# Performance work log

Hardware: AMD Instinct MI355X
Metric: run time of the kernel (lower is better)

Reference implementation:

```python
import jax, jax.numpy as jnp
import numpy as np

OFFSET_SCALE = 6.0
B, H, W = 128, 256, 256


def setup_inputs() -> dict:
    key = jax.random.key(0)
    k1, k2, k3, k4 = jax.random.split(key, 4)
    Offset = jax.random.normal(k1, (B, 3, H, W), dtype=jnp.float32)
    Posmap_kpt = jax.random.normal(k2, (B, 3, H, W), dtype=jnp.float32)
    mean_posmap = jax.random.normal(k3, (3, H, W), dtype=jnp.float32)
    uv_kpt = jax.random.randint(k4, (68, 2), 0, 256, dtype=jnp.int64)
    return {"Offset": Offset, "Posmap_kpt": Posmap_kpt,
            "mean_posmap": mean_posmap, "uv_kpt": uv_kpt}


def _kpt2tform_batch(kpt_src, kpt_dst):
    # kpt_src, kpt_dst: (B, 68, 3). Index 33 is the nose-tip anchor.
    sd1 = jnp.sum(jnp.linalg.norm(kpt_src - kpt_src[:, 33:34], axis=2), axis=1)[:, None, None]
    sd2 = jnp.sum(jnp.linalg.norm(kpt_dst - kpt_dst[:, 33:34], axis=2), axis=1)[:, None, None]
    A = kpt_src * sd2 / sd1
    Bm = kpt_dst
    AA = A - A.mean(axis=1, keepdims=True)
    BB = Bm - Bm.mean(axis=1, keepdims=True)
    Hm = jnp.einsum('bki,bkj->bij', AA, BB)  # (B, 3, 3)
    U, S, Vh = jnp.linalg.svd(Hm, full_matrices=False)
    # torch.svd returns V with H = U S V^T; R = V @ U^T
    R = jnp.einsum('bji,bkj->bik', Vh, U)
    t = jnp.mean(Bm - jnp.einsum('bki,bji->bkj', A, R), axis=1)  # (B, 3)
    return R * sd2 / sd1, t


def reference(Offset, Posmap_kpt, mean_posmap, uv_kpt):
    b = Offset.shape[0]
    offsetmap = Offset * OFFSET_SCALE + mean_posmap            # (B, 3, 256, 256)
    offsetmap = jnp.transpose(offsetmap, (0, 2, 3, 1))          # (B, 256, 256, 3)
    kptmap = jnp.transpose(Posmap_kpt, (0, 2, 3, 1))
    kpt_dst = kptmap[:, uv_kpt[:, 0], uv_kpt[:, 1]]             # (B, 68, 3)
    kpt_src = offsetmap[:, uv_kpt[:, 0], uv_kpt[:, 1]]
    offs = offsetmap.reshape(b, H * W, 3)                       # (B, 65536, 3)
    R, T = _kpt2tform_batch(kpt_src, kpt_dst)
    outpos = jnp.einsum('bki,bji->bkj', offs, R) + T[:, None, :]
    outpos = outpos.reshape(b, H, W, 3)
    return jnp.transpose(outpos, (0, 3, 1, 2))
```

## Files before the change

kernel.cpp:

```cpp
#include <hip/hip_runtime.h>
#include <math.h>

#define BATCH 128
#define HH 256
#define WW 256
#define HW (HH * WW)
#define HW4 (HW / 4)
#define NKPT 68

__device__ inline double wave_sum64(double v) {
#pragma unroll
    for (int off = 32; off > 0; off >>= 1) v += __shfl_xor(v, off);
    return v;
}

__global__ __launch_bounds__(64) void tform_kernel(
    const float* __restrict__ Offset, const float* __restrict__ Posmap,
    const float* __restrict__ meanp, const int* __restrict__ uv,
    float* __restrict__ RT) {
    const int b = blockIdx.x;
    const int lane = threadIdx.x;
    const float* offb = Offset + (size_t)b * 3 * HW;
    const float* dstb = Posmap + (size_t)b * 3 * HW;

    const bool has1 = lane < (NKPT - 64);

    double s0[3], d0[3], s1[3] = {0, 0, 0}, d1[3] = {0, 0, 0};
    {
        const int p0 = uv[lane * 2 + 0] * WW + uv[lane * 2 + 1];
#pragma unroll
        for (int i = 0; i < 3; i++) {
            s0[i] = (double)offb[(size_t)i * HW + p0] * 6.0 +
                    (double)meanp[(size_t)i * HW + p0];
            d0[i] = (double)dstb[(size_t)i * HW + p0];
        }
        if (has1) {
            const int k1 = lane + 64;
            const int p1 = uv[k1 * 2 + 0] * WW + uv[k1 * 2 + 1];
#pragma unroll
            for (int i = 0; i < 3; i++) {
                s1[i] = (double)offb[(size_t)i * HW + p1] * 6.0 +
                        (double)meanp[(size_t)i * HW + p1];
                d1[i] = (double)dstb[(size_t)i * HW + p1];
            }
        }
    }

    double s33[3], d33[3];
#pragma unroll
    for (int i = 0; i < 3; i++) {
        s33[i] = __shfl(s0[i], 33);
        d33[i] = __shfl(d0[i], 33);
    }

    double ns0 = 0, nd0 = 0, ns1 = 0, nd1 = 0;
    double ssum[3], dsum[3];
#pragma unroll
    for (int i = 0; i < 3; i++) {
        double es = s0[i] - s33[i], ed = d0[i] - d33[i];
        ns0 += es * es;
        nd0 += ed * ed;
        es = s1[i] - s33[i];
        ed = d1[i] - d33[i];
        ns1 += es * es;
        nd1 += ed * ed;
        ssum[i] = s0[i] + s1[i];
        dsum[i] = d0[i] + d1[i];
    }
    double sd1p = sqrt(ns0) + (has1 ? sqrt(ns1) : 0.0);
    double sd2p = sqrt(nd0) + (has1 ? sqrt(nd1) : 0.0);

    const double sd1 = wave_sum64(sd1p);
    const double sd2 = wave_sum64(sd2p);
#pragma unroll
    for (int i = 0; i < 3; i++) {
        ssum[i] = wave_sum64(ssum[i]);
        dsum[i] = wave_sum64(dsum[i]);
    }

    const double s = sd2 / sd1;
    double sbar[3], dbar[3];
#pragma unroll
    for (int i = 0; i < 3; i++) {
        sbar[i] = ssum[i] / NKPT;
        dbar[i] = dsum[i] / NKPT;
    }

    double Hm[3][3];
    {
        double aa0[3], bb0[3], aa1[3], bb1[3];
#pragma unroll
        for (int i = 0; i < 3; i++) {
            aa0[i] = (s0[i] - sbar[i]) * s;
            bb0[i] = d0[i] - dbar[i];
            aa1[i] = has1 ? (s1[i] - sbar[i]) * s : 0.0;
            bb1[i] = has1 ? (d1[i] - dbar[i]) : 0.0;
        }
#pragma unroll
        for (int i = 0; i < 3; i++)
#pragma unroll
            for (int j = 0; j < 3; j++)
                Hm[i][j] = wave_sum64(aa0[i] * bb0[j] + aa1[i] * bb1[j]);
    }

    if (lane != 0) return;

    double A[3][3];
    for (int i = 0; i < 3; i++)
        for (int j = 0; j < 3; j++) {
            double acc = 0;
            for (int kk = 0; kk < 3; kk++) acc += Hm[kk][i] * Hm[kk][j];
            A[i][j] = acc;
        }

    double V[3][3] = {{1, 0, 0}, {0, 1, 0}, {0, 0, 1}};
    for (int sweep = 0; sweep < 12; ++sweep) {
        double off = fabs(A[0][1]) + fabs(A[0][2]) + fabs(A[1][2]);
        double diag = fabs(A[0][0]) + fabs(A[1][1]) + fabs(A[2][2]);
        if (off <= diag * 1e-15) break;
        for (int p = 0; p < 2; p++)
            for (int q = p + 1; q < 3; q++) {
                double apq = A[p][q];
                if (fabs(apq) < 1e-300) continue;
                double theta = (A[q][q] - A[p][p]) / (2.0 * apq);
                double t = (theta >= 0.0 ? 1.0 : -1.0) /
                           (fabs(theta) + sqrt(theta * theta + 1.0));
                double c = 1.0 / sqrt(t * t + 1.0);
                double sn = t * c;
                A[p][p] -= t * apq;
                A[q][q] += t * apq;
                A[p][q] = 0.0;
                A[q][p] = 0.0;
                int r = 3 - p - q;
                double arp = A[r][p], arq = A[r][q];
                A[r][p] = A[p][r] = c * arp - sn * arq;
                A[r][q] = A[q][r] = sn * arp + c * arq;
#pragma unroll
                for (int rr = 0; rr < 3; rr++) {
                    double vrp = V[rr][p], vrq = V[rr][q];
                    V[rr][p] = c * vrp - sn * vrq;
                    V[rr][q] = sn * vrp + c * vrq;
                }
            }
    }
    double isig[3];
#pragma unroll
    for (int i = 0; i < 3; i++) {
        double l = A[i][i];
        if (l < 1e-30) l = 1e-30;
        isig[i] = 1.0 / sqrt(l);
    }
    double Wm[3][3];
    for (int i = 0; i < 3; i++)
        for (int j = 0; j < 3; j++) {
            double acc = 0;
            for (int kk = 0; kk < 3; kk++) acc += V[i][kk] * V[j][kk] * isig[kk];
            Wm[i][j] = acc;
        }
    double R[3][3];
    for (int i = 0; i < 3; i++)
        for (int j = 0; j < 3; j++) {
            double acc = 0;
            for (int kk = 0; kk < 3; kk++) acc += Wm[i][kk] * Hm[j][kk];
            R[i][j] = acc;
        }

    float* rt = RT + b * 12;
    for (int j = 0; j < 3; j++) {
        for (int i = 0; i < 3; i++) rt[j * 3 + i] = (float)(R[j][i] * s);
        double tj = dbar[j];
        for (int i = 0; i < 3; i++) tj -= s * sbar[i] * R[j][i];
        rt[9 + j] = (float)tj;
    }
}

__global__ __launch_bounds__(256) void apply_kernel(
    const float4* __restrict__ Off, const float4* __restrict__ Mean,
    const float* __restrict__ RT, float4* __restrict__ Out) {
    const int CHUNKS = HW4 / 256;
    const int b = blockIdx.x / CHUNKS;
    const int p = (blockIdx.x % CHUNKS) * 256 + threadIdx.x;

    const float* rt = RT + b * 12;
    const float r00 = rt[0], r01 = rt[1], r02 = rt[2];
    const float r10 = rt[3], r11 = rt[4], r12 = rt[5];
    const float r20 = rt[6], r21 = rt[7], r22 = rt[8];
    const float t0 = rt[9], t1 = rt[10], t2 = rt[11];

    const size_t base = (size_t)b * 3 * HW4;
    float4 o0 = Off[base + p];
    float4 o1 = Off[base + HW4 + p];
    float4 o2 = Off[base + 2 * HW4 + p];
    float4 m0 = Mean[p];
    float4 m1 = Mean[HW4 + p];
    float4 m2 = Mean[2 * HW4 + p];

    float4 y0, y1, y2;
#define APPLY(comp)                                                   \
    {                                                                 \
        float x0 = fmaf(o0.comp, 6.0f, m0.comp);                      \
        float x1 = fmaf(o1.comp, 6.0f, m1.comp);                      \
        float x2 = fmaf(o2.comp, 6.0f, m2.comp);                      \
        y0.comp = fmaf(x0, r00, fmaf(x1, r01, fmaf(x2, r02, t0)));    \
        y1.comp = fmaf(x0, r10, fmaf(x1, r11, fmaf(x2, r12, t1)));    \
        y2.comp = fmaf(x0, r20, fmaf(x1, r21, fmaf(x2, r22, t2)));    \
    }
    APPLY(x)
    APPLY(y)
    APPLY(z)
    APPLY(w)
#undef APPLY

    Out[base + p] = y0;
    Out[base + HW4 + p] = y1;
    Out[base + 2 * HW4 + p] = y2;
}

extern "C" void kernel_launch(void* const* d_in, const int* in_sizes, int n_in,
                              void* d_out, int out_size, void* d_ws,
                              size_t ws_size, hipStream_t stream) {
    const float* Offset = (const float*)d_in[0];
    const float* Posmap = (const float*)d_in[1];
    const float* meanp = (const float*)d_in[2];
    const int* uv = (const int*)d_in[3];
    float* out = (float*)d_out;
    float* RT = (float*)d_ws;

    tform_kernel<<<BATCH, 64, 0, stream>>>(Offset, Posmap, meanp, uv, RT);
    apply_kernel<<<BATCH * (HW4 / 256), 256, 0, stream>>>(
        (const float4*)Offset, (const float4*)meanp, RT, (float4*)out);
}
```

Baseline: 44.00 us.

## Fuse per-batch transform solve into apply kernel with redundant per-block computation

Merges the two kernels into one. Every 256-thread block now recomputes the batch's Procrustes transform in its first wave (keypoint gather, wave reductions, Jacobi SVD on lane 0) and passes it to the rest of the block through shared memory. The block's Offset loads are issued before the solve so they overlap it. The change also switches the output writes to nontemporal stores. It removes the second launch and the workspace round trip, but repeats the serial double-precision solve 64 times per batch and makes every block wait at a barrier for it.

Result: slower. 83.73 us (+90.3%).

```diff
diff --git a/kernel.cpp b/kernel.cpp
--- a/kernel.cpp
+++ b/kernel.cpp
@@ -6,7 +6,10 @@
 #define WW 256
 #define HW (HH * WW)
 #define HW4 (HW / 4)
+#define CHUNKS (HW4 / 256)
 #define NKPT 68
+
+typedef float fx4 __attribute__((ext_vector_type(4)));
 
 __device__ inline double wave_sum64(double v) {
 #pragma unroll
@@ -14,206 +17,202 @@
     return v;
 }
 
-__global__ __launch_bounds__(64) void tform_kernel(
+__global__ __launch_bounds__(256, 4) void fused_kernel(
     const float* __restrict__ Offset, const float* __restrict__ Posmap,
     const float* __restrict__ meanp, const int* __restrict__ uv,
-    float* __restrict__ RT) {
-    const int b = blockIdx.x;
-    const int lane = threadIdx.x;
-    const float* offb = Offset + (size_t)b * 3 * HW;
-    const float* dstb = Posmap + (size_t)b * 3 * HW;
-
-    const bool has1 = lane < (NKPT - 64);
-
-    double s0[3], d0[3], s1[3] = {0, 0, 0}, d1[3] = {0, 0, 0};
-    {
-        const int p0 = uv[lane * 2 + 0] * WW + uv[lane * 2 + 1];
-#pragma unroll
-        for (int i = 0; i < 3; i++) {
-            s0[i] = (double)offb[(size_t)i * HW + p0] * 6.0 +
-                    (double)meanp[(size_t)i * HW + p0];
-            d0[i] = (double)dstb[(size_t)i * HW + p0];
-        }
-        if (has1) {
-            const int k1 = lane + 64;
-            const int p1 = uv[k1 * 2 + 0] * WW + uv[k1 * 2 + 1];
-#pragma unroll
-            for (int i = 0; i < 3; i++) {
-                s1[i] = (double)offb[(size_t)i * HW + p1] * 6.0 +
-                        (double)meanp[(size_t)i * HW + p1];
-                d1[i] = (double)dstb[(size_t)i * HW + p1];
-            }
-        }
-    }
-
-    double s33[3], d33[3];
-#pragma unroll
-    for (int i = 0; i < 3; i++) {
-        s33[i] = __shfl(s0[i], 33);
-        d33[i] = __shfl(d0[i], 33);
-    }
-
-    double ns0 = 0, nd0 = 0, ns1 = 0, nd1 = 0;
-    double ssum[3], dsum[3];
-#pragma unroll
-    for (int i = 0; i < 3; i++) {
-        double es = s0[i] - s33[i], ed = d0[i] - d33[i];
-        ns0 += es * es;
-        nd0 += ed * ed;
-        es = s1[i] - s33[i];
-        ed = d1[i] - d33[i];
-        ns1 += es * es;
-        nd1 += ed * ed;
-        ssum[i] = s0[i] + s1[i];
-        dsum[i] = d0[i] + d1[i];
-    }
-    double sd1p = sqrt(ns0) + (has1 ? sqrt(ns1) : 0.0);
-    double sd2p = sqrt(nd0) + (has1 ? sqrt(nd1) : 0.0);
-
-    const double sd1 = wave_sum64(sd1p);
-    const double sd2 = wave_sum64(sd2p);
-#pragma unroll
-    for (int i = 0; i < 3; i++) {
-        ssum[i] = wave_sum64(ssum[i]);
-        dsum[i] = wave_sum64(dsum[i]);
-    }
-
-    const double s = sd2 / sd1;
-    double sbar[3], dbar[3];
-#pragma unroll
-    for (int i = 0; i < 3; i++) {
-        sbar[i] = ssum[i] / NKPT;
-        dbar[i] = dsum[i] / NKPT;
-    }
-
-    double Hm[3][3];
-    {
-        double aa0[3], bb0[3], aa1[3], bb1[3];
-#pragma unroll
-        for (int i = 0; i < 3; i++) {
-            aa0[i] = (s0[i] - sbar[i]) * s;
-            bb0[i] = d0[i] - dbar[i];
-            aa1[i] = has1 ? (s1[i] - sbar[i]) * s : 0.0;
-            bb1[i] = has1 ? (d1[i] - dbar[i]) : 0.0;
-        }
-#pragma unroll
-        for (int i = 0; i < 3; i++)
-#pragma unroll
-            for (int j = 0; j < 3; j++)
-                Hm[i][j] = wave_sum64(aa0[i] * bb0[j] + aa1[i] * bb1[j]);
-    }
-
-    if (lane != 0) return;
-
-    double A[3][3];
-    for (int i = 0; i < 3; i++)
-        for (int j = 0; j < 3; j++) {
-            double acc = 0;
-            for (int kk = 0; kk < 3; kk++) acc += Hm[kk][i] * Hm[kk][j];
-            A[i][j] = acc;
-        }
-
-    double V[3][3] = {{1, 0, 0}, {0, 1, 0}, {0, 0, 1}};
-    for (int sweep = 0; sweep < 12; ++sweep) {
-        double off = fabs(A[0][1]) + fabs(A[0][2]) + fabs(A[1][2]);
-        double diag = fabs(A[0][0]) + fabs(A[1][1]) + fabs(A[2][2]);
-        if (off <= diag * 1e-15) break;
-        for (int p = 0; p < 2; p++)
-            for (int q = p + 1; q < 3; q++) {
-                double apq = A[p][q];
-                if (fabs(apq) < 1e-300) continue;
-                double theta = (A[q][q] - A[p][p]) / (2.0 * apq);
-                double t = (theta >= 0.0 ? 1.0 : -1.0) /
-                           (fabs(theta) + sqrt(theta * theta + 1.0));
-                double c = 1.0 / sqrt(t * t + 1.0);
-                double sn = t * c;
-                A[p][p] -= t * apq;
-                A[q][q] += t * apq;
-                A[p][q] = 0.0;
-                A[q][p] = 0.0;
-                int r = 3 - p - q;
-                double arp = A[r][p], arq = A[r][q];
-                A[r][p] = A[p][r] = c * arp - sn * arq;
-                A[r][q] = A[q][r] = sn * arp + c * arq;
-#pragma unroll
-                for (int rr = 0; rr < 3; rr++) {
-                    double vrp = V[rr][p], vrq = V[rr][q];
-                    V[rr][p] = c * vrp - sn * vrq;
-                    V[rr][q] = sn * vrp + c * vrq;
-                }
-            }
-    }
-    double isig[3];
-#pragma unroll
-    for (int i = 0; i < 3; i++) {
-        double l = A[i][i];
-        if (l < 1e-30) l = 1e-30;
-        isig[i] = 1.0 / sqrt(l);
-    }
-    double Wm[3][3];
-    for (int i = 0; i < 3; i++)
-        for (int j = 0; j < 3; j++) {
-            double acc = 0;
-            for (int kk = 0; kk < 3; kk++) acc += V[i][kk] * V[j][kk] * isig[kk];
-            Wm[i][j] = acc;
-        }
-    double R[3][3];
-    for (int i = 0; i < 3; i++)
-        for (int j = 0; j < 3; j++) {
-            double acc = 0;
-            for (int kk = 0; kk < 3; kk++) acc += Wm[i][kk] * Hm[j][kk];
-            R[i][j] = acc;
-        }
-
-    float* rt = RT + b * 12;
-    for (int j = 0; j < 3; j++) {
-        for (int i = 0; i < 3; i++) rt[j * 3 + i] = (float)(R[j][i] * s);
-        double tj = dbar[j];
-        for (int i = 0; i < 3; i++) tj -= s * sbar[i] * R[j][i];
-        rt[9 + j] = (float)tj;
-    }
-}
-
-__global__ __launch_bounds__(256) void apply_kernel(
-    const float4* __restrict__ Off, const float4* __restrict__ Mean,
-    const float* __restrict__ RT, float4* __restrict__ Out) {
-    const int CHUNKS = HW4 / 256;
+    float* __restrict__ Out) {
+    __shared__ float rt_s[12];
+
     const int b = blockIdx.x / CHUNKS;
     const int p = (blockIdx.x % CHUNKS) * 256 + threadIdx.x;
-
-    const float* rt = RT + b * 12;
-    const float r00 = rt[0], r01 = rt[1], r02 = rt[2];
-    const float r10 = rt[3], r11 = rt[4], r12 = rt[5];
-    const float r20 = rt[6], r21 = rt[7], r22 = rt[8];
-    const float t0 = rt[9], t1 = rt[10], t2 = rt[11];
-
-    const size_t base = (size_t)b * 3 * HW4;
-    float4 o0 = Off[base + p];
-    float4 o1 = Off[base + HW4 + p];
-    float4 o2 = Off[base + 2 * HW4 + p];
-    float4 m0 = Mean[p];
-    float4 m1 = Mean[HW4 + p];
-    float4 m2 = Mean[2 * HW4 + p];
-
-    float4 y0, y1, y2;
-#define APPLY(comp)                                                   \
-    {                                                                 \
-        float x0 = fmaf(o0.comp, 6.0f, m0.comp);                      \
-        float x1 = fmaf(o1.comp, 6.0f, m1.comp);                      \
-        float x2 = fmaf(o2.comp, 6.0f, m2.comp);                      \
-        y0.comp = fmaf(x0, r00, fmaf(x1, r01, fmaf(x2, r02, t0)));    \
-        y1.comp = fmaf(x0, r10, fmaf(x1, r11, fmaf(x2, r12, t1)));    \
-        y2.comp = fmaf(x0, r20, fmaf(x1, r21, fmaf(x2, r22, t2)));    \
+    const size_t base4 = (size_t)b * 3 * HW4;
+
+    const fx4* Off4 = (const fx4*)Offset;
+    fx4 o0 = Off4[base4 + p];
+    fx4 o1 = Off4[base4 + HW4 + p];
+    fx4 o2 = Off4[base4 + 2 * HW4 + p];
+
+    if (threadIdx.x < 64) {
+        const int lane = threadIdx.x;
+        const float* offb = Offset + (size_t)b * 3 * HW;
+        const float* dstb = Posmap + (size_t)b * 3 * HW;
+        const bool has1 = lane < (NKPT - 64);
+
+        double s0[3], d0[3], s1[3] = {0, 0, 0}, d1[3] = {0, 0, 0};
+        {
+            const int p0 = uv[lane * 2 + 0] * WW + uv[lane * 2 + 1];
+#pragma unroll
+            for (int i = 0; i < 3; i++) {
+                s0[i] = (double)offb[(size_t)i * HW + p0] * 6.0 +
+                        (double)meanp[(size_t)i * HW + p0];
+                d0[i] = (double)dstb[(size_t)i * HW + p0];
+            }
+            if (has1) {
+                const int k1 = lane + 64;
+                const int p1 = uv[k1 * 2 + 0] * WW + uv[k1 * 2 + 1];
+#pragma unroll
+                for (int i = 0; i < 3; i++) {
+                    s1[i] = (double)offb[(size_t)i * HW + p1] * 6.0 +
+                            (double)meanp[(size_t)i * HW + p1];
+                    d1[i] = (double)dstb[(size_t)i * HW + p1];
+                }
+            }
+        }
+
+        double s33[3], d33[3];
+#pragma unroll
+        for (int i = 0; i < 3; i++) {
+            s33[i] = __shfl(s0[i], 33);
+            d33[i] = __shfl(d0[i], 33);
+        }
+
+        double ns0 = 0, nd0 = 0, ns1 = 0, nd1 = 0;
+        double ssum[3], dsum[3];
+#pragma unroll
+        for (int i = 0; i < 3; i++) {
+            double es = s0[i] - s33[i], ed = d0[i] - d33[i];
+            ns0 += es * es;
+            nd0 += ed * ed;
+            es = s1[i] - s33[i];
+            ed = d1[i] - d33[i];
+            ns1 += es * es;
+            nd1 += ed * ed;
+            ssum[i] = s0[i] + s1[i];
+            dsum[i] = d0[i] + d1[i];
+        }
+        double sd1p = sqrt(ns0) + (has1 ? sqrt(ns1) : 0.0);
+        double sd2p = sqrt(nd0) + (has1 ? sqrt(nd1) : 0.0);
+
+        const double sd1 = wave_sum64(sd1p);
+        const double sd2 = wave_sum64(sd2p);
+#pragma unroll
+        for (int i = 0; i < 3; i++) {
+            ssum[i] = wave_sum64(ssum[i]);
+            dsum[i] = wave_sum64(dsum[i]);
+        }
+
+        const double s = sd2 / sd1;
+        double sbar[3], dbar[3];
+#pragma unroll
+        for (int i = 0; i < 3; i++) {
+            sbar[i] = ssum[i] / NKPT;
+            dbar[i] = dsum[i] / NKPT;
+        }
+
+        double Hm[3][3];
+        {
+            double aa0[3], bb0[3], aa1[3], bb1[3];
+#pragma unroll
+            for (int i = 0; i < 3; i++) {
+                aa0[i] = (s0[i] - sbar[i]) * s;
+                bb0[i] = d0[i] - dbar[i];
+                aa1[i] = has1 ? (s1[i] - sbar[i]) * s : 0.0;
+                bb1[i] = has1 ? (d1[i] - dbar[i]) : 0.0;
+            }
+#pragma unroll
+            for (int i = 0; i < 3; i++)
+#pragma unroll
+                for (int j = 0; j < 3; j++)
+                    Hm[i][j] = wave_sum64(aa0[i] * bb0[j] + aa1[i] * bb1[j]);
+        }
+
+        if (lane == 0) {
+            double A[3][3];
+            for (int i = 0; i < 3; i++)
+                for (int j = 0; j < 3; j++) {
+                    double acc = 0;
+                    for (int kk = 0; kk < 3; kk++) acc += Hm[kk][i] * Hm[kk][j];
+                    A[i][j] = acc;
+                }
+
+            double V[3][3] = {{1, 0, 0}, {0, 1, 0}, {0, 0, 1}};
+            for (int sweep = 0; sweep < 12; ++sweep) {
+                double off = fabs(A[0][1]) + fabs(A[0][2]) + fabs(A[1][2]);
+                double diag = fabs(A[0][0]) + fabs(A[1][1]) + fabs(A[2][2]);
+                if (off <= diag * 1e-15) break;
+                for (int pp = 0; pp < 2; pp++)
+                    for (int q = pp + 1; q < 3; q++) {
+                        double apq = A[pp][q];
+                        if (fabs(apq) < 1e-300) continue;
+                        double theta = (A[q][q] - A[pp][pp]) / (2.0 * apq);
+                        double t = (theta >= 0.0 ? 1.0 : -1.0) /
+                                   (fabs(theta) + sqrt(theta * theta + 1.0));
+                        double c = 1.0 / sqrt(t * t + 1.0);
+                        double sn = t * c;
+                        A[pp][pp] -= t * apq;
+                        A[q][q] += t * apq;
+                        A[pp][q] = 0.0;
+                        A[q][pp] = 0.0;
+                        int r = 3 - pp - q;
+                        double arp = A[r][pp], arq = A[r][q];
+                        A[r][pp] = A[pp][r] = c * arp - sn * arq;
+                        A[r][q] = A[q][r] = sn * arp + c * arq;
+#pragma unroll
+                        for (int rr = 0; rr < 3; rr++) {
+                            double vrp = V[rr][pp], vrq = V[rr][q];
+                            V[rr][pp] = c * vrp - sn * vrq;
+                            V[rr][q] = sn * vrp + c * vrq;
+                        }
+                    }
+            }
+            double isig[3];
+#pragma unroll
+            for (int i = 0; i < 3; i++) {
+                double l = A[i][i];
+                if (l < 1e-30) l = 1e-30;
+                isig[i] = 1.0 / sqrt(l);
+            }
+            double Wm[3][3];
+            for (int i = 0; i < 3; i++)
+                for (int j = 0; j < 3; j++) {
+                    double acc = 0;
+                    for (int kk = 0; kk < 3; kk++)
+                        acc += V[i][kk] * V[j][kk] * isig[kk];
+                    Wm[i][j] = acc;
+                }
+            double R[3][3];
+            for (int i = 0; i < 3; i++)
+                for (int j = 0; j < 3; j++) {
+                    double acc = 0;
+                    for (int kk = 0; kk < 3; kk++) acc += Wm[i][kk] * Hm[j][kk];
+                    R[i][j] = acc;
+                }
+            for (int j = 0; j < 3; j++) {
+                for (int i = 0; i < 3; i++)
+                    rt_s[j * 3 + i] = (float)(R[j][i] * s);
+                double tj = dbar[j];
+                for (int i = 0; i < 3; i++) tj -= s * sbar[i] * R[j][i];
+                rt_s[9 + j] = (float)tj;
+            }
+        }
     }
-    APPLY(x)
-    APPLY(y)
-    APPLY(z)
-    APPLY(w)
-#undef APPLY
-
-    Out[base + p] = y0;
-    Out[base + HW4 + p] = y1;
-    Out[base + 2 * HW4 + p] = y2;
+    __syncthreads();
+
+    const float r00 = rt_s[0], r01 = rt_s[1], r02 = rt_s[2];
+    const float r10 = rt_s[3], r11 = rt_s[4], r12 = rt_s[5];
+    const float r20 = rt_s[6], r21 = rt_s[7], r22 = rt_s[8];
+    const float t0 = rt_s[9], t1 = rt_s[10], t2 = rt_s[11];
+
+    const fx4* Mean4 = (const fx4*)meanp;
+    fx4 m0 = Mean4[p];
+    fx4 m1 = Mean4[HW4 + p];
+    fx4 m2 = Mean4[2 * HW4 + p];
+
+    fx4 y0, y1, y2;
+#pragma unroll
+    for (int c = 0; c < 4; c++) {
+        float x0 = fmaf(o0[c], 6.0f, m0[c]);
+        float x1 = fmaf(o1[c], 6.0f, m1[c]);
+        float x2 = fmaf(o2[c], 6.0f, m2[c]);
+        y0[c] = fmaf(x0, r00, fmaf(x1, r01, fmaf(x2, r02, t0)));
+        y1[c] = fmaf(x0, r10, fmaf(x1, r11, fmaf(x2, r12, t1)));
+        y2[c] = fmaf(x0, r20, fmaf(x1, r21, fmaf(x2, r22, t2)));
+    }
+
+    fx4* Out4 = (fx4*)Out;
+    __builtin_nontemporal_store(y0, &Out4[base4 + p]);
+    __builtin_nontemporal_store(y1, &Out4[base4 + HW4 + p]);
+    __builtin_nontemporal_store(y2, &Out4[base4 + 2 * HW4 + p]);
 }
 
 extern "C" void kernel_launch(void* const* d_in, const int* in_sizes, int n_in,
@@ -224,9 +223,7 @@
     const float* meanp = (const float*)d_in[2];
     const int* uv = (const int*)d_in[3];
     float* out = (float*)d_out;
-    float* RT = (float*)d_ws;
-
-    tform_kernel<<<BATCH, 64, 0, stream>>>(Offset, Posmap, meanp, uv, RT);
-    apply_kernel<<<BATCH * (HW4 / 256), 256, 0, stream>>>(
-        (const float4*)Offset, (const float4*)meanp, RT, (float4*)out);
+
+    fused_kernel<<<BATCH * CHUNKS, 256, 0, stream>>>(Offset, Posmap, meanp, uv,
+                                                     out);
 }
```
